# Kernel optimization log

Measured on AMD Instinct MI355X. Metric: run time of the kernel, lower is better.

The kernel has to match this reference:

```python
import jax, jax.numpy as jnp
import numpy as np

J = 17
MIN_TORSO_H = 10.0
MAX_RANGE = 5.0
EPS = 1e-6
LN_EPS = 1e-5
LS, RS, LH, RH = 5, 6, 11, 12  # COCO shoulder/hip indices


def _mid(pl, pr, cl, cr):
    # conf-weighted midpoint: both valid -> mean, one valid -> that one, none -> 0
    wl = (cl > 0).astype(pl.dtype)[:, None]
    wr = (cr > 0).astype(pr.dtype)[:, None]
    s = wl * pl + wr * pr
    w = wl + wr
    return s / jnp.maximum(w, 1.0)


def torso_centric(kp):
    pos = kp[..., :2]          # [B, J, 2]
    conf = kp[..., 2:3]        # [B, J, 1]
    sc = conf[:, [LS, RS], 0]  # [B, 2]
    hc = conf[:, [LH, RH], 0]
    use_torso = ((sc > 0).sum(1) >= 1) & ((hc > 0).sum(1) >= 1)  # [B]
    sm = _mid(pos[:, LS], pos[:, RS], sc[:, 0], sc[:, 1])  # [B, 2]
    hm = _mid(pos[:, LH], pos[:, RH], hc[:, 0], hc[:, 1])
    sm = jnp.where(use_torso[:, None], sm, 0.0)
    hm = jnp.where(use_torso[:, None], hm, 0.0)
    center = (sm + hm) * 0.5                                   # [B, 2]
    height = jnp.linalg.norm(sm - hm, axis=1, keepdims=True)   # [B, 1]
    valid = use_torso & (height[:, 0] >= MIN_TORSO_H)
    torso_np = jnp.clip((pos - center[:, None, :]) / (height[:, None, :] + EPS),
                        -MAX_RANGE, MAX_RANGE)
    # bbox fallback (bbox computed from keypoints)
    mn = pos.min(axis=1, keepdims=True)
    mx = pos.max(axis=1, keepdims=True)
    bbox_np = jnp.clip((pos - mn) / (mx - mn + EPS), -MAX_RANGE, MAX_RANGE)
    norm_pos = jnp.where(valid[:, None, None], torso_np, bbox_np)
    return jnp.concatenate([norm_pos, conf], axis=-1)


def _ln(x, g, b):
    m = x.mean(-1, keepdims=True)
    v = ((x - m) ** 2).mean(-1, keepdims=True)
    return (x - m) / jnp.sqrt(v + LN_EPS) * g + b


def setup_inputs() -> dict:
    key = jax.random.key(0)
    ks = jax.random.split(key, 24)
    B = 32768

    def mk_kp(k0, k1, k2):
        pos = jax.random.uniform(k0, (B, J, 2)) * 512.0
        conf = jax.random.uniform(k1, (B, J, 1))
        conf = jnp.where(jax.random.uniform(k2, (B, J, 1)) < 0.2, 0.0, conf)
        return jnp.concatenate([pos, conf], -1)

    inp = {
        'keypoints': mk_kp(ks[0], ks[1], ks[2]),
        'prev_keypoints': mk_kp(ks[3], ks[4], ks[5]),
        'joint_emb': jax.random.normal(ks[6], (J, 16)) * 0.05,
        'pos_W': jax.random.normal(ks[7], (2, 16)) * 0.05, 'pos_b': jnp.zeros((16,)),
        'vel_W': jax.random.normal(ks[8], (2, 8)) * 0.05, 'vel_b': jnp.zeros((8,)),
        'angvel_W': jax.random.normal(ks[9], (3, 8)) * 0.05, 'angvel_b': jnp.zeros((8,)),
        'rel_W': jax.random.normal(ks[10], (2, 8)) * 0.05, 'rel_b': jnp.zeros((8,)),
        'conf_W': jax.random.normal(ks[11], (1, 4)) * 0.05, 'conf_b': jnp.zeros((4,)),
        'p1_W': jax.random.normal(ks[12], (60, 128)) * 0.05, 'p1_b': jnp.zeros((128,)),
        'ln1_g': jnp.ones((128,)), 'ln1_b': jnp.zeros((128,)),
        'p2_W': jax.random.normal(ks[13], (128, 64)) * 0.05, 'p2_b': jnp.zeros((64,)),
        'ln2_g': jnp.ones((64,)), 'ln2_b': jnp.zeros((64,)),
    }
    return inp


def reference(keypoints, prev_keypoints, joint_emb,
              pos_W, pos_b, vel_W, vel_b, angvel_W, angvel_b,
              rel_W, rel_b, conf_W, conf_b,
              p1_W, p1_b, ln1_g, ln1_b, p2_W, p2_b, ln2_g, ln2_b):
    B = keypoints.shape[0]
    kp = torso_centric(keypoints)
    pkp = torso_centric(prev_keypoints)
    pos = kp[..., :2]
    conf = kp[..., 2:3]

    type_emb = jnp.broadcast_to(joint_emb[None], (B, J, 16))
    pos_emb = pos @ pos_W + pos_b                               # [B,J,16]
    vel = pos - pkp[..., :2]
    vel_emb = vel @ vel_W + vel_b                               # [B,J,8]
    # use_angles=False -> angular velocities are zeros through the encoder
    angvel_emb = jnp.broadcast_to(angvel_b[None, None], (B, J, 8))
    # relative position to torso center (mean of shoulder/hip joints)
    torso_center = pos[:, jnp.array([LS, RS, LH, RH])].mean(axis=1, keepdims=True)
    rel_emb = (pos - torso_center) @ rel_W + rel_b              # [B,J,8]
    conf_emb = conf @ conf_W + conf_b                           # [B,J,4]

    feats = jnp.concatenate([type_emb, pos_emb, vel_emb, angvel_emb,
                             rel_emb, conf_emb], axis=-1)       # [B,J,60]
    h = _ln(feats @ p1_W + p1_b, ln1_g, ln1_b)
    h = jax.nn.relu(h)                                          # dropout is identity (eval)
    out = _ln(h @ p2_W + p2_b, ln2_g, ln2_b)                    # [B,J,64]
    return out
```

## Files before the change

kernel.cpp:

```cpp
#include <hip/hip_runtime.h>
#include <hip/hip_bf16.h>

#define NJ 17
#define ROWS 32
#define TPB 256
#define TOKPB (ROWS * NJ)

#define LSJ 5
#define RSJ 6
#define LHJ 11
#define RHJ 12

#define WS_A1   16384
#define WS_G1P  24576
#define WS_B1P  24832
#define WS_LN2  25088
#define WS_U32  6464
#define WS_CHNK 1616

typedef __attribute__((ext_vector_type(8))) short bf16x8;
typedef __attribute__((ext_vector_type(8))) _Float16 f16x8;
typedef __attribute__((ext_vector_type(2))) _Float16 f16x2;
typedef __attribute__((ext_vector_type(4))) float f32x4;
typedef __attribute__((ext_vector_type(4))) unsigned int u32x4;

__device__ __forceinline__ unsigned short f2hu(float x) {
    _Float16 h = (_Float16)x;
    return __builtin_bit_cast(unsigned short, h);
}
__device__ __forceinline__ f16x2 cvt2h(float lo, float hi) {
    return __builtin_bit_cast(f16x2, __builtin_amdgcn_cvt_pkrtz(lo, hi));
}

__device__ __forceinline__ float row16_sum(float s) {
    int t;
    t = __builtin_amdgcn_update_dpp(0, __builtin_bit_cast(int, s), 0x121, 0xf, 0xf, true);
    s += __builtin_bit_cast(float, t);
    t = __builtin_amdgcn_update_dpp(0, __builtin_bit_cast(int, s), 0x122, 0xf, 0xf, true);
    s += __builtin_bit_cast(float, t);
    t = __builtin_amdgcn_update_dpp(0, __builtin_bit_cast(int, s), 0x124, 0xf, 0xf, true);
    s += __builtin_bit_cast(float, t);
    t = __builtin_amdgcn_update_dpp(0, __builtin_bit_cast(int, s), 0x128, 0xf, 0xf, true);
    s += __builtin_bit_cast(float, t);
    return s;
}

__device__ __forceinline__ void norm_row(const float* __restrict__ r,
                                         float* __restrict__ ox,
                                         float* __restrict__ oy) {
    float sc0 = r[LSJ*3+2], sc1 = r[RSJ*3+2];
    float hc0 = r[LHJ*3+2], hc1 = r[RHJ*3+2];
    bool ut = ((sc0 > 0.f) || (sc1 > 0.f)) && ((hc0 > 0.f) || (hc1 > 0.f));

    float wl = sc0 > 0.f ? 1.f : 0.f;
    float wr = sc1 > 0.f ? 1.f : 0.f;
    float ws = fmaxf(wl + wr, 1.f);
    float smx = (wl * r[LSJ*3+0] + wr * r[RSJ*3+0]) / ws;
    float smy = (wl * r[LSJ*3+1] + wr * r[RSJ*3+1]) / ws;

    wl = hc0 > 0.f ? 1.f : 0.f;
    wr = hc1 > 0.f ? 1.f : 0.f;
    ws = fmaxf(wl + wr, 1.f);
    float hmx = (wl * r[LHJ*3+0] + wr * r[RHJ*3+0]) / ws;
    float hmy = (wl * r[LHJ*3+1] + wr * r[RHJ*3+1]) / ws;

    if (!ut) { smx = 0.f; smy = 0.f; hmx = 0.f; hmy = 0.f; }

    float cx = (smx + hmx) * 0.5f;
    float cy = (smy + hmy) * 0.5f;
    float dx = smx - hmx, dy = smy - hmy;
    float hh = sqrtf(dx * dx + dy * dy);
    bool valid = ut && (hh >= 10.0f);

    float mnx = r[0], mxx = r[0], mny = r[1], mxy = r[1];
    #pragma unroll
    for (int j = 1; j < NJ; ++j) {
        float x = r[j*3], y = r[j*3+1];
        mnx = fminf(mnx, x); mxx = fmaxf(mxx, x);
        mny = fminf(mny, y); mxy = fmaxf(mxy, y);
    }

    float ih  = 1.f / (hh + 1e-6f);
    float ibx = 1.f / (mxx - mnx + 1e-6f);
    float iby = 1.f / (mxy - mny + 1e-6f);

    #pragma unroll
    for (int j = 0; j < NJ; ++j) {
        float x = r[j*3], y = r[j*3+1];
        float tx = (x - cx) * ih, ty = (y - cy) * ih;
        float bx = (x - mnx) * ibx, by = (y - mny) * iby;
        float nx = valid ? tx : bx;
        float ny = valid ? ty : by;
        ox[j] = fminf(fmaxf(nx, -5.f), 5.f);
        oy[j] = fminf(fmaxf(ny, -5.f), 5.f);
    }
}

__global__ __launch_bounds__(256) void setup_kernel(
    const float* __restrict__ emb,
    const float* __restrict__ posW, const float* __restrict__ posB,
    const float* __restrict__ velW, const float* __restrict__ velB,
    const float* __restrict__ angB,
    const float* __restrict__ relW, const float* __restrict__ relB,
    const float* __restrict__ confW, const float* __restrict__ confB,
    const float* __restrict__ P1, const float* __restrict__ p1b,
    const float* __restrict__ g1, const float* __restrict__ b1,
    const float* __restrict__ W2, const float* __restrict__ p2b,
    const float* __restrict__ g2, const float* __restrict__ b2,
    unsigned int* __restrict__ ws)
{
    __shared__ float sPA[7][128];
    __shared__ float sBase[128];
    __shared__ float sK0[17][128];
    const int tid = threadIdx.x;

    if (tid < 128) {
        const int n = tid;
        float pa0 = 0.f, pa1 = 0.f;
        #pragma unroll
        for (int i = 0; i < 16; ++i) {
            float w = P1[(16 + i) * 128 + n];
            pa0 += posW[i] * w; pa1 += posW[16 + i] * w;
        }
        float pv0 = 0.f, pv1 = 0.f;
        #pragma unroll
        for (int i = 0; i < 8; ++i) {
            float w = P1[(32 + i) * 128 + n];
            pv0 += velW[i] * w; pv1 += velW[8 + i] * w;
        }
        float pr0 = 0.f, pr1 = 0.f;
        #pragma unroll
        for (int i = 0; i < 8; ++i) {
            float w = P1[(48 + i) * 128 + n];
            pr0 += relW[i] * w; pr1 += relW[8 + i] * w;
        }
        float pc = 0.f;
        #pragma unroll
        for (int i = 0; i < 4; ++i) pc += confW[i] * P1[(56 + i) * 128 + n];

        float base = p1b[n];
        #pragma unroll
        for (int i = 0; i < 16; ++i) base += posB[i]  * P1[(16 + i) * 128 + n];
        #pragma unroll
        for (int i = 0; i < 8; ++i)  base += velB[i]  * P1[(32 + i) * 128 + n];
        #pragma unroll
        for (int i = 0; i < 8; ++i)  base += angB[i]  * P1[(40 + i) * 128 + n];
        #pragma unroll
        for (int i = 0; i < 8; ++i)  base += relB[i]  * P1[(48 + i) * 128 + n];
        #pragma unroll
        for (int i = 0; i < 4; ++i)  base += confB[i] * P1[(56 + i) * 128 + n];

        sPA[0][n] = pa0; sPA[1][n] = pa1;
        sPA[2][n] = pv0; sPA[3][n] = pv1;
        sPA[4][n] = pr0; sPA[5][n] = pr1;
        sPA[6][n] = pc;  sBase[n] = base;
    } else {
        const int t = tid - 128;
        const int n = t & 63;
        const int gp = (t >> 6) * 2;
        const unsigned xm = (unsigned)(n & 15) << 4;
        #pragma unroll
        for (int dg = 0; dg < 2; ++dg) {
            const int gg = gp + dg;
            #pragma unroll
            for (int ks = 0; ks < 4; ++ks) {
                unsigned int pk[4];
                #pragma unroll
                for (int ep = 0; ep < 4; ++ep) {
                    int e0 = 2 * ep, e1 = 2 * ep + 1;
                    int c0 = 4 * gg + (e0 & 3) + 16 * (2 * ks + (e0 >> 2));
                    int c1 = 4 * gg + (e1 & 3) + 16 * (2 * ks + (e1 >> 2));
                    unsigned lo = f2hu(W2[c0 * 64 + n]);
                    unsigned hi = f2hu(W2[c1 * 64 + n]);
                    pk[ep] = lo | (hi << 16);
                }
                unsigned byte = (unsigned)n * 256u + ((unsigned)((ks * 4 + gg) * 16) ^ xm);
                *(u32x4*)&ws[byte >> 2] = (u32x4){pk[0], pk[1], pk[2], pk[3]};
            }
        }
    }

    if (tid < 32) {
        const int gg = tid >> 3, nt1 = tid & 7;
        const int c0 = 4 * gg + 16 * nt1;
        ws[(WS_G1P >> 2) + tid * 2 + 0] = (unsigned)f2hu(g1[c0+0]) | ((unsigned)f2hu(g1[c0+1]) << 16);
        ws[(WS_G1P >> 2) + tid * 2 + 1] = (unsigned)f2hu(g1[c0+2]) | ((unsigned)f2hu(g1[c0+3]) << 16);
        ws[(WS_B1P >> 2) + tid * 2 + 0] = (unsigned)f2hu(b1[c0+0]) | ((unsigned)f2hu(b1[c0+1]) << 16);
        ws[(WS_B1P >> 2) + tid * 2 + 1] = (unsigned)f2hu(b1[c0+2]) | ((unsigned)f2hu(b1[c0+3]) << 16);
    } else if (tid >= 64 && tid < 256) {
        const int i = tid - 64;
        float v = (i < 64) ? g2[i] : (i < 128 ? b2[i - 64] : p2b[i - 128]);
        ws[(WS_LN2 >> 2) + i] = __builtin_bit_cast(unsigned, v);
    }
    __syncthreads();

    for (int e = tid; e < NJ * 128; e += 256) {
        int j = e >> 7, n = e & 127;
        float v = sBase[n];
        #pragma unroll
        for (int t = 0; t < 16; ++t) v += emb[j * 16 + t] * P1[t * 128 + n];
        sK0[j][n] = v;
    }
    __syncthreads();

    for (int i = tid; i < 512; i += 256) {
        const int nt1 = i >> 6, ln = i & 63, gg = ln >> 4, tl2 = ln & 15;
        const int ch = tl2 + 16 * nt1;
        float w[8];
        #pragma unroll
        for (int e = 0; e < 8; ++e) w[e] = 0.f;
        if (gg == 0) {
            #pragma unroll
            for (int e = 0; e < 7; ++e) w[e] = sPA[e][ch];
            w[7] = sK0[0][ch];
        } else if (gg == 1) {
            #pragma unroll
            for (int e = 0; e < 8; ++e) w[e] = sK0[e + 1][ch];
        } else if (gg == 2) {
            #pragma unroll
            for (int e = 0; e < 8; ++e) w[e] = sK0[e + 9][ch];
        }
        unsigned u[4];
        #pragma unroll
        for (int p = 0; p < 4; ++p) {
            unsigned short lo = f2hu(w[2*p]);
            unsigned short hi = f2hu(w[2*p+1]);
            u[p] = (unsigned)lo | ((unsigned)hi << 16);
        }
        *(u32x4*)&ws[(WS_A1 >> 2) + i * 4] = (u32x4){u[0], u[1], u[2], u[3]};
    }
}

__global__ __launch_bounds__(TPB, 2)
void jfe_kernel(
    const float* __restrict__ kp, const float* __restrict__ pkp,
    const unsigned int* __restrict__ ws,
    float* __restrict__ out, int B)
{
    __shared__ __align__(16) unsigned int sWS[WS_U32];
    __shared__ __align__(16) float4 sPk[TOKPB];
    __shared__ __align__(8)  float2 sQ[TOKPB];
    __shared__ float2 sTc[ROWS];
    __shared__ __align__(16) float sXp[4][4][80];

    const int tid  = threadIdx.x;
    const int lane = tid & 63;
    const int wv   = tid >> 6;
    const int g    = lane >> 4;
    const int tl   = lane & 15;

    const int row0  = blockIdx.x * ROWS;
    const int nrows = min(ROWS, B - row0);
    const long long tok0 = (long long)blockIdx.x * TOKPB;
    const long long ntok = (long long)B * NJ;

    for (int c = tid; c < WS_CHNK; c += TPB) {
        u32x4 t = *(const u32x4*)&ws[c * 4];
        *(u32x4*)&sWS[c * 4] = t;
    }

    if (tl < 16 && g == 0) {
        const int task  = wv * 16 + tl;
        const int frame = task >> 5;
        const int row   = task & 31;
        if (row < nrows) {
            float ox[NJ], oy[NJ];
            if (frame == 0) {
                const float* rp = kp + (long long)(row0 + row) * 51;
                norm_row(rp, ox, oy);
                #pragma unroll
                for (int j = 0; j < NJ; ++j)
                    sPk[row * NJ + j] = make_float4(ox[j], oy[j], rp[j * 3 + 2], 0.f);
                sTc[row] = make_float2(
                    0.25f * (ox[LSJ] + ox[RSJ] + ox[LHJ] + ox[RHJ]),
                    0.25f * (oy[LSJ] + oy[RSJ] + oy[LHJ] + oy[RHJ]));
            } else {
                norm_row(pkp + (long long)(row0 + row) * 51, ox, oy);
                #pragma unroll
                for (int j = 0; j < NJ; ++j)
                    sQ[row * NJ + j] = make_float2(ox[j], oy[j]);
            }
        }
    }
    __syncthreads();

    f16x8 a1f[8];
    #pragma unroll
    for (int nt1 = 0; nt1 < 8; ++nt1)
        a1f[nt1] = __builtin_bit_cast(f16x8,
            *(const u32x4*)&sWS[(WS_A1 >> 2) + (nt1 * 64 + lane) * 4]);

    f16x2 g1h[8][2], b1h[8][2];
    #pragma unroll
    for (int nt1 = 0; nt1 < 8; ++nt1) {
        g1h[nt1][0] = __builtin_bit_cast(f16x2, sWS[(WS_G1P >> 2) + (g * 8 + nt1) * 2 + 0]);
        g1h[nt1][1] = __builtin_bit_cast(f16x2, sWS[(WS_G1P >> 2) + (g * 8 + nt1) * 2 + 1]);
        b1h[nt1][0] = __builtin_bit_cast(f16x2, sWS[(WS_B1P >> 2) + (g * 8 + nt1) * 2 + 0]);
        b1h[nt1][1] = __builtin_bit_cast(f16x2, sWS[(WS_B1P >> 2) + (g * 8 + nt1) * 2 + 1]);
    }
    float g2v[4], b2v[4], p2v[4];
    #pragma unroll
    for (int nt = 0; nt < 4; ++nt) {
        g2v[nt] = __builtin_bit_cast(float, sWS[(WS_LN2 >> 2) +   0 + 4 * tl + nt]);
        b2v[nt] = __builtin_bit_cast(float, sWS[(WS_LN2 >> 2) +  64 + 4 * tl + nt]);
        p2v[nt] = __builtin_bit_cast(float, sWS[(WS_LN2 >> 2) + 128 + nt * 16 + tl]);
    }

    const int ntiles = (nrows * NJ + 15) >> 4;
    const unsigned xm = (unsigned)tl << 4;
    #pragma unroll 1
    for (int t = wv; t < ntiles; t += 4) {
        const int tbase = t * 16;
        const int tok = tbase + tl;
        const int r = (tok * 3856) >> 16;
        const int j = tok - r * NJ;

        const float4 pk = sPk[tok];
        const float2 qv = sQ[tok];
        const float2 tc = sTc[r];
        const float px = pk.x, py = pk.y, cf = pk.z;
        const float vx = px - qv.x, vy = py - qv.y;
        const float rx = px - tc.x, ry = py - tc.y;

        f16x8 bf;
        {
            const int base7 = g * 8 - 7;
            #pragma unroll
            for (int e = 0; e < 8; ++e) {
                float oh = ((base7 + e) == j) ? 1.f : 0.f;
                float val;
                if (e == 0) val = (g == 0) ? px : oh;
                else if (e == 1) val = (g == 0) ? py : oh;
                else if (e == 2) val = (g == 0) ? vx : oh;
                else if (e == 3) val = (g == 0) ? vy : oh;
                else if (e == 4) val = (g == 0) ? rx : oh;
                else if (e == 5) val = (g == 0) ? ry : oh;
                else if (e == 6) val = (g == 0) ? cf : oh;
                else val = oh;
                bf[e] = (_Float16)val;
            }
        }

        f32x4 acc1[8];
        #pragma unroll
        for (int nt1 = 0; nt1 < 8; ++nt1)
            acc1[nt1] = __builtin_amdgcn_mfma_f32_16x16x32_f16(
                a1f[nt1], bf, (f32x4){0.f, 0.f, 0.f, 0.f}, 0, 0, 0);

        float s = 0.f, ss = 0.f;
        #pragma unroll
        for (int nt1 = 0; nt1 < 8; ++nt1)
            #pragma unroll
            for (int q = 0; q < 4; ++q) { float v = acc1[nt1][q]; s += v; ss += v * v; }
        s += __shfl_xor(s, 16); ss += __shfl_xor(ss, 16);
        s += __shfl_xor(s, 32); ss += __shfl_xor(ss, 32);
        const float mu  = s * (1.f / 128.f);
        const float inv = rsqrtf(ss * (1.f / 128.f) - mu * mu + 1e-5f);

        const f16x2 im2 = cvt2h(inv, inv);
        const f16x2 nm2 = cvt2h(-mu * inv, -mu * inv);
        const f16x2 zero2 = (f16x2)(_Float16)0.f;
        u32x4 afu[4];
        #pragma unroll
        for (int nt1 = 0; nt1 < 8; ++nt1) {
            const int ks = nt1 >> 1, sl = 2 * (nt1 & 1);
            f16x2 a01 = cvt2h(acc1[nt1][0], acc1[nt1][1]);
            f16x2 a23 = cvt2h(acc1[nt1][2], acc1[nt1][3]);
            f16x2 s01 = g1h[nt1][0] * im2;
            f16x2 s23 = g1h[nt1][1] * im2;
            f16x2 c01 = g1h[nt1][0] * nm2 + b1h[nt1][0];
            f16x2 c23 = g1h[nt1][1] * nm2 + b1h[nt1][1];
            f16x2 t01 = __builtin_elementwise_max(a01 * s01 + c01, zero2);
            f16x2 t23 = __builtin_elementwise_max(a23 * s23 + c23, zero2);
            afu[ks][sl + 0] = __builtin_bit_cast(unsigned, t01);
            afu[ks][sl + 1] = __builtin_bit_cast(unsigned, t23);
        }

        f32x4 acc2[4];
        #pragma unroll
        for (int nt = 0; nt < 4; ++nt)
            acc2[nt] = (f32x4){p2v[nt], p2v[nt], p2v[nt], p2v[nt]};
        #pragma unroll
        for (int ks = 0; ks < 4; ++ks) {
            const unsigned so = ((unsigned)((ks * 4 + g) * 16) ^ xm) >> 2;
            const f16x8 afk = __builtin_bit_cast(f16x8, afu[ks]);
            #pragma unroll
            for (int nt = 0; nt < 4; ++nt) {
                const unsigned idx = (unsigned)(nt * 16 + tl) * 64u + so;
                f16x8 bw = __builtin_bit_cast(f16x8, *(const u32x4*)&sWS[idx]);
                acc2[nt] = __builtin_amdgcn_mfma_f32_16x16x32_f16(afk, bw, acc2[nt], 0, 0, 0);
            }
        }

        const long long gbase = tok0 + tbase;
        #pragma unroll
        for (int q = 0; q < 4; ++q) {
            float a0 = acc2[0][q], a1 = acc2[1][q], a2 = acc2[2][q], a3 = acc2[3][q];
            float s2 = row16_sum(a0 + a1 + a2 + a3);
            float q2 = row16_sum(a0*a0 + a1*a1 + a2*a2 + a3*a3);
            const long long gtok = gbase + g * 4 + q;
            const float mu2  = s2 * (1.f / 64.f);
            const float inv2 = rsqrtf(q2 * (1.f / 64.f) - mu2 * mu2 + 1e-5f);
            sXp[wv][g][ 0 + tl] = (a0 - mu2) * inv2;
            sXp[wv][g][16 + tl] = (a1 - mu2) * inv2;
            sXp[wv][g][32 + tl] = (a2 - mu2) * inv2;
            sXp[wv][g][48 + tl] = (a3 - mu2) * inv2;
            f32x4 w = *(const f32x4*)&sXp[wv][g][4 * tl];
            if (gtok < ntok) {
                f32x4 v;
                v[0] = w[0] * g2v[0] + b2v[0];
                v[1] = w[1] * g2v[1] + b2v[1];
                v[2] = w[2] * g2v[2] + b2v[2];
                v[3] = w[3] * g2v[3] + b2v[3];
                *(f32x4*)(out + gtok * 64 + 4 * tl) = v;
            }
        }
    }
}

extern "C" void kernel_launch(void* const* d_in, const int* in_sizes, int n_in,
                              void* d_out, int out_size, void* d_ws, size_t ws_size,
                              hipStream_t stream) {
    const float* kp    = (const float*)d_in[0];
    const float* pkp   = (const float*)d_in[1];
    const float* emb   = (const float*)d_in[2];
    const float* posW  = (const float*)d_in[3];
    const float* posB  = (const float*)d_in[4];
    const float* velW  = (const float*)d_in[5];
    const float* velB  = (const float*)d_in[6];
    const float* angB  = (const float*)d_in[8];
    const float* relW  = (const float*)d_in[9];
    const float* relB  = (const float*)d_in[10];
    const float* confW = (const float*)d_in[11];
    const float* confB = (const float*)d_in[12];
    const float* P1    = (const float*)d_in[13];
    const float* p1b   = (const float*)d_in[14];
    const float* g1    = (const float*)d_in[15];
    const float* b1    = (const float*)d_in[16];
    const float* W2    = (const float*)d_in[17];
    const float* p2b   = (const float*)d_in[18];
    const float* g2    = (const float*)d_in[19];
    const float* b2    = (const float*)d_in[20];
    float* out = (float*)d_out;
    unsigned int* ws = (unsigned int*)d_ws;

    int B = in_sizes[0] / (NJ * 3);

    setup_kernel<<<1, 256, 0, stream>>>(
        emb, posW, posB, velW, velB, angB, relW, relB, confW, confB,
        P1, p1b, g1, b1, W2, p2b, g2, b2, ws);

    int nblocks = (B + ROWS - 1) / ROWS;
    jfe_kernel<<<nblocks, TPB, 0, stream>>>(kp, pkp, ws, out, B);
}
```

Baseline: 57.64 us.

## Shrink shared memory by aliasing A1 staging with transpose scratch, compact workspace

Repacks the workspace layout so the A1 fragment lives in its own shared buffer. After it is loaded into registers, that buffer is reused as the per-wave transpose scratch for the LayerNorm-2 output, which drops the separate sXp array and lowers LDS per block. The output transpose now double-buffers two rows to overlap LDS writes and reads, and full blocks skip the bounds check. The LN sums are also rebalanced into tree reductions for more ILP. The trade-off is an extra block barrier and tighter coupling between buffer lifetimes.

```diff
diff --git a/kernel.cpp b/kernel.cpp
--- a/kernel.cpp
+++ b/kernel.cpp
@@ -11,12 +11,13 @@
 #define LHJ 11
 #define RHJ 12
 
-#define WS_A1   16384
-#define WS_G1P  24576
-#define WS_B1P  24832
-#define WS_LN2  25088
-#define WS_U32  6464
-#define WS_CHNK 1616
+#define WSU_A1   4096
+#define WSU_PRM  6144
+
+#define SH_G1P  4096
+#define SH_B1P  4160
+#define SH_LN2  4224
+#define SH_U32  4416
 
 typedef __attribute__((ext_vector_type(8))) short bf16x8;
 typedef __attribute__((ext_vector_type(8))) _Float16 f16x8;
@@ -183,14 +184,14 @@
     if (tid < 32) {
         const int gg = tid >> 3, nt1 = tid & 7;
         const int c0 = 4 * gg + 16 * nt1;
-        ws[(WS_G1P >> 2) + tid * 2 + 0] = (unsigned)f2hu(g1[c0+0]) | ((unsigned)f2hu(g1[c0+1]) << 16);
-        ws[(WS_G1P >> 2) + tid * 2 + 1] = (unsigned)f2hu(g1[c0+2]) | ((unsigned)f2hu(g1[c0+3]) << 16);
-        ws[(WS_B1P >> 2) + tid * 2 + 0] = (unsigned)f2hu(b1[c0+0]) | ((unsigned)f2hu(b1[c0+1]) << 16);
-        ws[(WS_B1P >> 2) + tid * 2 + 1] = (unsigned)f2hu(b1[c0+2]) | ((unsigned)f2hu(b1[c0+3]) << 16);
+        ws[WSU_PRM + tid * 2 + 0]      = (unsigned)f2hu(g1[c0+0]) | ((unsigned)f2hu(g1[c0+1]) << 16);
+        ws[WSU_PRM + tid * 2 + 1]      = (unsigned)f2hu(g1[c0+2]) | ((unsigned)f2hu(g1[c0+3]) << 16);
+        ws[WSU_PRM + 64 + tid * 2 + 0] = (unsigned)f2hu(b1[c0+0]) | ((unsigned)f2hu(b1[c0+1]) << 16);
+        ws[WSU_PRM + 64 + tid * 2 + 1] = (unsigned)f2hu(b1[c0+2]) | ((unsigned)f2hu(b1[c0+3]) << 16);
     } else if (tid >= 64 && tid < 256) {
         const int i = tid - 64;
         float v = (i < 64) ? g2[i] : (i < 128 ? b2[i - 64] : p2b[i - 128]);
-        ws[(WS_LN2 >> 2) + i] = __builtin_bit_cast(unsigned, v);
+        ws[WSU_PRM + 128 + i] = __builtin_bit_cast(unsigned, v);
     }
     __syncthreads();
 
@@ -227,7 +228,7 @@
             unsigned short hi = f2hu(w[2*p+1]);
             u[p] = (unsigned)lo | ((unsigned)hi << 16);
         }
-        *(u32x4*)&ws[(WS_A1 >> 2) + i * 4] = (u32x4){u[0], u[1], u[2], u[3]};
+        *(u32x4*)&ws[WSU_A1 + i * 4] = (u32x4){u[0], u[1], u[2], u[3]};
     }
 }
 
@@ -237,11 +238,11 @@
     const unsigned int* __restrict__ ws,
     float* __restrict__ out, int B)
 {
-    __shared__ __align__(16) unsigned int sWS[WS_U32];
+    __shared__ __align__(16) unsigned int sWS[SH_U32];
+    __shared__ __align__(16) unsigned int sA1[2176];
     __shared__ __align__(16) float4 sPk[TOKPB];
     __shared__ __align__(8)  float2 sQ[TOKPB];
     __shared__ float2 sTc[ROWS];
-    __shared__ __align__(16) float sXp[4][4][80];
 
     const int tid  = threadIdx.x;
     const int lane = tid & 63;
@@ -254,10 +255,12 @@
     const long long tok0 = (long long)blockIdx.x * TOKPB;
     const long long ntok = (long long)B * NJ;
 
-    for (int c = tid; c < WS_CHNK; c += TPB) {
-        u32x4 t = *(const u32x4*)&ws[c * 4];
-        *(u32x4*)&sWS[c * 4] = t;
-    }
+    for (int c = tid; c < 1024; c += TPB)
+        *(u32x4*)&sWS[c * 4] = *(const u32x4*)&ws[c * 4];
+    for (int c = tid; c < 512; c += TPB)
+        *(u32x4*)&sA1[c * 4] = *(const u32x4*)&ws[WSU_A1 + c * 4];
+    if (tid < 80)
+        *(u32x4*)&sWS[SH_G1P + tid * 4] = *(const u32x4*)&ws[WSU_PRM + tid * 4];
 
     if (tl < 16 && g == 0) {
         const int task  = wv * 16 + tl;
@@ -288,26 +291,31 @@
     #pragma unroll
     for (int nt1 = 0; nt1 < 8; ++nt1)
         a1f[nt1] = __builtin_bit_cast(f16x8,
-            *(const u32x4*)&sWS[(WS_A1 >> 2) + (nt1 * 64 + lane) * 4]);
+            *(const u32x4*)&sA1[(nt1 * 64 + lane) * 4]);
 
     f16x2 g1h[8][2], b1h[8][2];
     #pragma unroll
     for (int nt1 = 0; nt1 < 8; ++nt1) {
-        g1h[nt1][0] = __builtin_bit_cast(f16x2, sWS[(WS_G1P >> 2) + (g * 8 + nt1) * 2 + 0]);
-        g1h[nt1][1] = __builtin_bit_cast(f16x2, sWS[(WS_G1P >> 2) + (g * 8 + nt1) * 2 + 1]);
-        b1h[nt1][0] = __builtin_bit_cast(f16x2, sWS[(WS_B1P >> 2) + (g * 8 + nt1) * 2 + 0]);
-        b1h[nt1][1] = __builtin_bit_cast(f16x2, sWS[(WS_B1P >> 2) + (g * 8 + nt1) * 2 + 1]);
+        g1h[nt1][0] = __builtin_bit_cast(f16x2, sWS[SH_G1P + (g * 8 + nt1) * 2 + 0]);
+        g1h[nt1][1] = __builtin_bit_cast(f16x2, sWS[SH_G1P + (g * 8 + nt1) * 2 + 1]);
+        b1h[nt1][0] = __builtin_bit_cast(f16x2, sWS[SH_B1P + (g * 8 + nt1) * 2 + 0]);
+        b1h[nt1][1] = __builtin_bit_cast(f16x2, sWS[SH_B1P + (g * 8 + nt1) * 2 + 1]);
     }
     float g2v[4], b2v[4], p2v[4];
     #pragma unroll
     for (int nt = 0; nt < 4; ++nt) {
-        g2v[nt] = __builtin_bit_cast(float, sWS[(WS_LN2 >> 2) +   0 + 4 * tl + nt]);
-        b2v[nt] = __builtin_bit_cast(float, sWS[(WS_LN2 >> 2) +  64 + 4 * tl + nt]);
-        p2v[nt] = __builtin_bit_cast(float, sWS[(WS_LN2 >> 2) + 128 + nt * 16 + tl]);
-    }
-
+        g2v[nt] = __builtin_bit_cast(float, sWS[SH_LN2 +   0 + 4 * tl + nt]);
+        b2v[nt] = __builtin_bit_cast(float, sWS[SH_LN2 +  64 + 4 * tl + nt]);
+        p2v[nt] = __builtin_bit_cast(float, sWS[SH_LN2 + 128 + nt * 16 + tl]);
+    }
+    __syncthreads();
+
+    float* const sXp = (float*)sA1 + wv * 544 + g * 136;
+
+    const bool full = (nrows == ROWS);
     const int ntiles = (nrows * NJ + 15) >> 4;
     const unsigned xm = (unsigned)tl << 4;
+
     #pragma unroll 1
     for (int t = wv; t < ntiles; t += 4) {
         const int tbase = t * 16;
@@ -347,11 +355,19 @@
             acc1[nt1] = __builtin_amdgcn_mfma_f32_16x16x32_f16(
                 a1f[nt1], bf, (f32x4){0.f, 0.f, 0.f, 0.f}, 0, 0, 0);
 
-        float s = 0.f, ss = 0.f;
-        #pragma unroll
-        for (int nt1 = 0; nt1 < 8; ++nt1)
-            #pragma unroll
-            for (int q = 0; q < 4; ++q) { float v = acc1[nt1][q]; s += v; ss += v * v; }
+        float s, ss;
+        {
+            float t0[8], t1[8];
+            #pragma unroll
+            for (int n1 = 0; n1 < 8; ++n1) {
+                float a0 = acc1[n1][0], a1 = acc1[n1][1];
+                float a2 = acc1[n1][2], a3 = acc1[n1][3];
+                t0[n1] = (a0 + a1) + (a2 + a3);
+                t1[n1] = (a0 * a0 + a1 * a1) + (a2 * a2 + a3 * a3);
+            }
+            s  = ((t0[0] + t0[1]) + (t0[2] + t0[3])) + ((t0[4] + t0[5]) + (t0[6] + t0[7]));
+            ss = ((t1[0] + t1[1]) + (t1[2] + t1[3])) + ((t1[4] + t1[5]) + (t1[6] + t1[7]));
+        }
         s += __shfl_xor(s, 16); ss += __shfl_xor(ss, 16);
         s += __shfl_xor(s, 32); ss += __shfl_xor(ss, 32);
         const float mu  = s * (1.f / 128.f);
@@ -392,29 +408,44 @@
             }
         }
 
-        const long long gbase = tok0 + tbase;
+        float vm[4], vi[4];
         #pragma unroll
         for (int q = 0; q < 4; ++q) {
             float a0 = acc2[0][q], a1 = acc2[1][q], a2 = acc2[2][q], a3 = acc2[3][q];
-            float s2 = row16_sum(a0 + a1 + a2 + a3);
-            float q2 = row16_sum(a0*a0 + a1*a1 + a2*a2 + a3*a3);
-            const long long gtok = gbase + g * 4 + q;
-            const float mu2  = s2 * (1.f / 64.f);
-            const float inv2 = rsqrtf(q2 * (1.f / 64.f) - mu2 * mu2 + 1e-5f);
-            sXp[wv][g][ 0 + tl] = (a0 - mu2) * inv2;
-            sXp[wv][g][16 + tl] = (a1 - mu2) * inv2;
-            sXp[wv][g][32 + tl] = (a2 - mu2) * inv2;
-            sXp[wv][g][48 + tl] = (a3 - mu2) * inv2;
-            f32x4 w = *(const f32x4*)&sXp[wv][g][4 * tl];
-            if (gtok < ntok) {
-                f32x4 v;
-                v[0] = w[0] * g2v[0] + b2v[0];
-                v[1] = w[1] * g2v[1] + b2v[1];
-                v[2] = w[2] * g2v[2] + b2v[2];
-                v[3] = w[3] * g2v[3] + b2v[3];
-                *(f32x4*)(out + gtok * 64 + 4 * tl) = v;
-            }
-        }
+            float s2 = row16_sum((a0 + a1) + (a2 + a3));
+            float q2 = row16_sum((a0 * a0 + a1 * a1) + (a2 * a2 + a3 * a3));
+            vm[q] = s2 * (1.f / 64.f);
+            vi[q] = rsqrtf(q2 * (1.f / 64.f) - vm[q] * vm[q] + 1e-5f);
+        }
+        float* const obase = out + (((long long)(tok0 + tbase) + g * 4) << 6) + 4 * tl;
+
+#define WRQ(q, rr) { \
+        float* d = sXp + (rr) * 68; \
+        d[ 0 + tl] = (acc2[0][q] - vm[q]) * vi[q]; \
+        d[16 + tl] = (acc2[1][q] - vm[q]) * vi[q]; \
+        d[32 + tl] = (acc2[2][q] - vm[q]) * vi[q]; \
+        d[48 + tl] = (acc2[3][q] - vm[q]) * vi[q]; }
+#define RDQ(q, rr) { \
+        f32x4 w = *(const f32x4*)&sXp[(rr) * 68 + 4 * tl]; \
+        f32x4 v; \
+        v[0] = w[0] * g2v[0] + b2v[0]; v[1] = w[1] * g2v[1] + b2v[1]; \
+        v[2] = w[2] * g2v[2] + b2v[2]; v[3] = w[3] * g2v[3] + b2v[3]; \
+        *(f32x4*)(obase + (q) * 64) = v; }
+#define RDQG(q, rr) { \
+        if (tok0 + tbase + g * 4 + (q) < ntok) RDQ(q, rr) }
+
+        if (full) {
+            WRQ(0, 0); WRQ(1, 1); RDQ(0, 0);
+            WRQ(2, 0); RDQ(1, 1);
+            WRQ(3, 1); RDQ(2, 0); RDQ(3, 1);
+        } else {
+            WRQ(0, 0); WRQ(1, 1); RDQG(0, 0);
+            WRQ(2, 0); RDQG(1, 1);
+            WRQ(3, 1); RDQG(2, 0); RDQG(3, 1);
+        }
+#undef WRQ
+#undef RDQ
+#undef RDQG
     }
 }
 
```

After: 59.61 us. 1.03x slower.
